# Kernel tuning notes

Measured on AMD Instinct MI355X. Metric: run time of the kernel, lower is better.

## Reference

```python
import jax, jax.numpy as jnp
import numpy as np
import math

M, N, D = 16384, 8192, 128
SIGMA = 1.0

def setup_inputs() -> dict:
    key = jax.random.key(0)
    k1, k2, k3 = jax.random.split(key, 3)
    x = jax.random.normal(k1, (M, D), dtype=jnp.float32)
    means = jax.random.normal(k2, (N, D), dtype=jnp.float32)
    weights = jax.random.uniform(k3, (N,), dtype=jnp.float32)
    return {"x": x, "means": means, "weights": weights}

def reference(x, means, weights):
    # GMM.eval_batch: cdist -> square -> gaussian kernel -> weighted sum
    var = SIGMA ** 2
    x = x.reshape(-1, means.shape[-1])
    x2 = jnp.sum(x * x, axis=-1, keepdims=True)            # (M,1)
    m2 = jnp.sum(means * means, axis=-1)                   # (N,)
    sq = jnp.maximum(x2 + m2[None, :] - 2.0 * (x @ means.T), 0.0)  # (M,N)
    coef = 1.0 / (2.0 * math.pi * var)
    dens = coef * jnp.exp(-sq / (2.0 * var))               # (M,N)
    return dens @ weights                                  # (M,)
```

## Files before the change

### kernel.cpp

```cpp
#include <hip/hip_runtime.h>
#include <math.h>

#define MM 16384
#define NN 8192
#define DD 128

#define L2E  1.4426950408889634f
#define COEF 0.15915494309189535f

__device__ __forceinline__ unsigned short f2h(float f) {
    _Float16 h = (_Float16)f;
    unsigned short u;
    __builtin_memcpy(&u, &h, 2);
    return u;
}

typedef __attribute__((ext_vector_type(8))) _Float16 f16x8;
typedef __attribute__((ext_vector_type(4))) float f32x4;

__global__ __launch_bounds__(256) void gmm_prep_f16(
    const float* __restrict__ x, const float* __restrict__ means,
    const float* __restrict__ w, short* __restrict__ Acat,
    short* __restrict__ Bcat, float* __restrict__ xc, float* __restrict__ mc)
{
    const int tid  = threadIdx.x;
    const int rbk  = blockIdx.x;
    const bool isx = rbk < (MM / 16);
    const int rb   = isx ? rbk : rbk - (MM / 16);
    const int lane = tid & 63;
    const int rp   = (tid >> 6) * 4 + (lane >> 4);
    const int cg   = lane & 15;
    const int p    = cg >> 2;
    const int gk   = cg & 3;
    const int row  = rb * 16 + rp;

    const float* src = (isx ? x : means) + (size_t)row * DD + cg * 8;
    float4 u0 = ((const float4*)src)[0];
    float4 u1 = ((const float4*)src)[1];
    float a[8] = {u0.x, u0.y, u0.z, u0.w, u1.x, u1.y, u1.z, u1.w};

    float ss = 0.f;
    unsigned hi[4];
    #pragma unroll
    for (int q = 0; q < 4; ++q) {
        ss = fmaf(a[2 * q], a[2 * q], fmaf(a[2 * q + 1], a[2 * q + 1], ss));
        float a0 = isx ? a[2 * q] * L2E     : a[2 * q];
        float a1 = isx ? a[2 * q + 1] * L2E : a[2 * q + 1];
        hi[q] = (unsigned)f2h(a0) | ((unsigned)f2h(a1) << 16);
    }
    uint4 HI = make_uint4(hi[0], hi[1], hi[2], hi[3]);

    const int slot = rp * 4 + ((gk + (rp >> 1)) & 3);
    short* base = (isx ? Acat : Bcat) + (size_t)rb * 2048 + p * 512 + slot * 8;
    *(uint4*)base = HI;

    ss += __shfl_xor(ss, 1, 16);
    ss += __shfl_xor(ss, 2, 16);
    ss += __shfl_xor(ss, 4, 16);
    ss += __shfl_xor(ss, 8, 16);
    if (cg == 0) {
        if (isx) xc[row] = -0.5f * ss * L2E;
        else     mc[row] = (logf(w[row]) - 0.5f * ss) * L2E;
    }
}

__global__ __launch_bounds__(256, 3) void gmm_mfma(
    const short* __restrict__ Acat, const short* __restrict__ Bcat,
    const float* __restrict__ xc, const float* __restrict__ mc,
    float* __restrict__ out)
{
    const int tid  = threadIdx.x;
    const int w    = tid >> 6, lane = tid & 63;
    const int wm   = w >> 1,   wn   = w & 1;
    const int quad = lane >> 4, col = lane & 15;
    const int m0   = blockIdx.x * 128;
    const int nb   = blockIdx.y * 128;

    const int rdo = col * 32 + ((quad + (col >> 1)) & 3) * 8;

    const short* ga = Acat + (size_t)(blockIdx.x * 8 + wm * 4) * 2048 + rdo;
    const short* gb = Bcat + (size_t)(blockIdx.y * 8 + wn * 4) * 2048 + rdo;

    float mcv[4];
    #pragma unroll
    for (int j = 0; j < 4; ++j) mcv[j] = mc[nb + wn * 64 + j * 16 + col];
    float xa[4][4];
    #pragma unroll
    for (int i = 0; i < 4; ++i) {
        float4 xv = *(const float4*)(xc + m0 + wm * 64 + i * 16 + quad * 4);
        xa[i][0] = xv.x; xa[i][1] = xv.y; xa[i][2] = xv.z; xa[i][3] = xv.w;
    }

    f32x4 acc[4][4];
    #pragma unroll
    for (int i = 0; i < 4; ++i)
        #pragma unroll
        for (int j = 0; j < 4; ++j)
            acc[i][j] = (f32x4){xa[i][0] + mcv[j], xa[i][1] + mcv[j],
                                xa[i][2] + mcv[j], xa[i][3] + mcv[j]};

    #pragma unroll
    for (int bk = 0; bk < 4; ++bk) {
        f16x8 af[4], bf[4];
        #pragma unroll
        for (int i = 0; i < 4; ++i)
            af[i] = *(const f16x8*)(ga + (size_t)i * 2048 + bk * 512);
        #pragma unroll
        for (int j = 0; j < 4; ++j)
            bf[j] = *(const f16x8*)(gb + (size_t)j * 2048 + bk * 512);
        #pragma unroll
        for (int j = 0; j < 4; ++j)
            #pragma unroll
            for (int i = 0; i < 4; ++i)
                acc[i][j] = __builtin_amdgcn_mfma_f32_16x16x32_f16(
                    af[i], bf[j], acc[i][j], 0, 0, 0);
    }

    #pragma unroll
    for (int i = 0; i < 4; ++i) {
        #pragma unroll
        for (int r = 0; r < 4; ++r) {
            float s = 0.f;
            #pragma unroll
            for (int j = 0; j < 4; ++j)
                s += __builtin_exp2f(acc[i][j][r]);
            s += __shfl_xor(s, 1, 16);
            s += __shfl_xor(s, 2, 16);
            s += __shfl_xor(s, 4, 16);
            s += __shfl_xor(s, 8, 16);
            if (col == 0)
                atomicAdd(out + m0 + wm * 64 + i * 16 + quad * 4 + r, COEF * s);
        }
    }
}

__global__ __launch_bounds__(256) void gmm_prep(
    const float* __restrict__ x, const float* __restrict__ means,
    const float* __restrict__ w, float* __restrict__ xc, float* __restrict__ mc)
{
    int tid = blockIdx.x * 256 + threadIdx.x;
    if (tid < MM) {
        const float4* row = (const float4*)(x + (size_t)tid * DD);
        float ss = 0.f;
        #pragma unroll
        for (int i = 0; i < DD / 4; ++i) {
            float4 v = row[i];
            ss = fmaf(v.x, v.x, fmaf(v.y, v.y, fmaf(v.z, v.z, fmaf(v.w, v.w, ss))));
        }
        xc[tid] = -0.5f * ss * L2E;
    } else if (tid < MM + NN) {
        int n = tid - MM;
        const float4* row = (const float4*)(means + (size_t)n * DD);
        float ss = 0.f;
        #pragma unroll
        for (int i = 0; i < DD / 4; ++i) {
            float4 v = row[i];
            ss = fmaf(v.x, v.x, fmaf(v.y, v.y, fmaf(v.z, v.z, fmaf(v.w, v.w, ss))));
        }
        mc[n] = (logf(w[n]) - 0.5f * ss) * L2E;
    }
}

__global__ __launch_bounds__(256, 2) void gmm_main(
    const float* __restrict__ x, const float* __restrict__ means,
    const float* __restrict__ xc, const float* __restrict__ mc,
    float* __restrict__ out)
{
    __shared__ __align__(16) float Asm[128 * 128];
    __shared__ __align__(16) float Bsm[2][16 * 128];

    const int t   = threadIdx.x;
    const int tc  = t & 15;
    const int tr  = t >> 4;
    const int r0  = blockIdx.x * 128;
    const int nq0 = blockIdx.y * 2048;

    {
        float4 tmp[16];
        #pragma unroll
        for (int ii = 0; ii < 16; ++ii) {
            int idx = t + ii * 256;
            int r   = idx >> 5;
            int k0  = (idx & 31) << 2;
            tmp[ii] = *(const float4*)(x + (size_t)(r0 + r) * DD + k0);
        }
        #pragma unroll
        for (int ii = 0; ii < 16; ++ii) {
            int idx = t + ii * 256;
            int r   = idx >> 5;
            int k0  = (idx & 31) << 2;
            int rb  = r >> 3, rl = r & 7;
            float v[4] = {tmp[ii].x, tmp[ii].y, tmp[ii].z, tmp[ii].w};
            #pragma unroll
            for (int j = 0; j < 4; ++j) {
                int k = k0 + j;
                Asm[k * 128 + (((rb ^ (k & 15)) << 3) | rl)] = v[j];
            }
        }
    }

    float xcv[8];
    {
        float4 a = *(const float4*)(xc + r0 + tr * 8);
        float4 b = *(const float4*)(xc + r0 + tr * 8 + 4);
        xcv[0] = a.x; xcv[1] = a.y; xcv[2] = a.z; xcv[3] = a.w;
        xcv[4] = b.x; xcv[5] = b.y; xcv[6] = b.z; xcv[7] = b.w;
    }

    float rowAcc[8];
    #pragma unroll
    for (int i = 0; i < 8; ++i) rowAcc[i] = 0.f;

    for (int ntile = 0; ntile < 16; ++ntile) {
        const int nbase = nq0 + ntile * 128;

        float acc[8][8];
        #pragma unroll
        for (int i = 0; i < 8; ++i)
            #pragma unroll
            for (int j = 0; j < 8; ++j) acc[i][j] = 0.f;

        float4 ld[2];
        #pragma unroll
        for (int ii = 0; ii < 2; ++ii) {
            int flat = t + ii * 256;
            int nl   = flat >> 2;
            int kl   = (flat & 3) << 2;
            ld[ii] = *(const float4*)(means + (size_t)(nbase + nl) * DD + kl);
        }

        for (int ks = 0; ks < 8; ++ks) {
            const int buf = ks & 1;
            #pragma unroll
            for (int ii = 0; ii < 2; ++ii) {
                int flat = t + ii * 256;
                int nl   = flat >> 2;
                int k0   = (flat & 3) << 2;
                int nbk  = nl >> 3, nll = nl & 7;
                float v[4] = {ld[ii].x, ld[ii].y, ld[ii].z, ld[ii].w};
                #pragma unroll
                for (int j = 0; j < 4; ++j) {
                    int kl = k0 + j;
                    Bsm[buf][kl * 128 + (((nbk ^ kl) << 3) | nll)] = v[j];
                }
            }
            if (ks < 7) {
                #pragma unroll
                for (int ii = 0; ii < 2; ++ii) {
                    int flat = t + ii * 256;
                    int nl   = flat >> 2;
                    int kl   = (flat & 3) << 2;
                    ld[ii] = *(const float4*)(means + (size_t)(nbase + nl) * DD
                                              + (ks + 1) * 16 + kl);
                }
            }
            __syncthreads();

            #pragma unroll
            for (int kk = 0; kk < 16; ++kk) {
                const int k = ks * 16 + kk;
                const float* apx = &Asm[k * 128 + ((tr ^ kk) << 3)];
                float4 a0 = *(const float4*)apx;
                float4 a1 = *(const float4*)(apx + 4);
                const float* bpx = &Bsm[buf][kk * 128 + ((tc ^ kk) << 3)];
                float4 b0 = *(const float4*)bpx;
                float4 b1 = *(const float4*)(bpx + 4);
                float av[8] = {a0.x, a0.y, a0.z, a0.w, a1.x, a1.y, a1.z, a1.w};
                float bv[8] = {b0.x, b0.y, b0.z, b0.w, b1.x, b1.y, b1.z, b1.w};
                #pragma unroll
                for (int i = 0; i < 8; ++i)
                    #pragma unroll
                    for (int j = 0; j < 8; ++j)
                        acc[i][j] = fmaf(av[i], bv[j], acc[i][j]);
            }
        }

        float mcv[8];
        {
            float4 a = *(const float4*)(mc + nbase + tc * 8);
            float4 b = *(const float4*)(mc + nbase + tc * 8 + 4);
            mcv[0] = a.x; mcv[1] = a.y; mcv[2] = a.z; mcv[3] = a.w;
            mcv[4] = b.x; mcv[5] = b.y; mcv[6] = b.z; mcv[7] = b.w;
        }
        #pragma unroll
        for (int i = 0; i < 8; ++i) {
            float s = 0.f;
            #pragma unroll
            for (int j = 0; j < 8; ++j) {
                float arg = fmaf(acc[i][j], L2E, xcv[i] + mcv[j]);
                s += __builtin_exp2f(arg);
            }
            rowAcc[i] += s;
        }
    }

    #pragma unroll
    for (int i = 0; i < 8; ++i) {
        float v = rowAcc[i];
        v += __shfl_xor(v, 1, 16);
        v += __shfl_xor(v, 2, 16);
        v += __shfl_xor(v, 4, 16);
        v += __shfl_xor(v, 8, 16);
        if (tc == 0) atomicAdd(out + r0 + tr * 8 + i, COEF * v);
    }
}

extern "C" void kernel_launch(void* const* d_in, const int* in_sizes, int n_in,
                              void* d_out, int out_size, void* d_ws, size_t ws_size,
                              hipStream_t stream) {
    const float* x     = (const float*)d_in[0];
    const float* means = (const float*)d_in[1];
    const float* w     = (const float*)d_in[2];
    float* out = (float*)d_out;

    const size_t needA = (size_t)MM * 128 * sizeof(short);
    const size_t needB = (size_t)NN * 128 * sizeof(short);
    const size_t need  = needA + needB + (size_t)(MM + NN) * 4;

    if (ws_size >= need) {
        short* Acat = (short*)d_ws;
        short* Bcat = Acat + (size_t)MM * 128;
        float* xc   = (float*)(Bcat + (size_t)NN * 128);
        float* mc   = xc + MM;
        hipMemsetAsync(out, 0, MM * sizeof(float), stream);
        gmm_prep_f16<<<(MM + NN) / 16, 256, 0, stream>>>(x, means, w, Acat, Bcat, xc, mc);
        gmm_mfma<<<dim3(MM / 128, NN / 128), 256, 0, stream>>>(Acat, Bcat, xc, mc, out);
    } else {
        float* xc = (float*)d_ws;
        float* mc = xc + MM;
        hipMemsetAsync(out, 0, MM * sizeof(float), stream);
        gmm_prep<<<(MM + NN + 255) / 256, 256, 0, stream>>>(x, means, w, xc, mc);
        gmm_main<<<dim3(MM / 128, 4), 256, 0, stream>>>(x, means, xc, mc, out);
    }
}
```

Before: 140.3 us.

## Stage MFMA operands through triple-buffered LDS with async global loads

The MFMA kernel now uses 512-thread blocks that each cover 128 rows by 1024 means. Operand chunks are streamed through a triple-buffered LDS ring filled by global_load_lds async copies, with vmcnt waits and barriers between stages. Per-row exp sums build up in registers across 8 N-tiles, which cuts the atomicAdd count by a factor of 8 and shares A/B tiles across waves. The cost is a block-wide barrier at every step, 48KB of LDS per block, and fewer blocks in the grid.

```diff
diff --git a/kernel.cpp b/kernel.cpp
--- a/kernel.cpp
+++ b/kernel.cpp
@@ -13,6 +13,13 @@
     unsigned short u;
     __builtin_memcpy(&u, &h, 2);
     return u;
+}
+
+__device__ __forceinline__ void async16(short* lds, const short* g) {
+    __builtin_amdgcn_global_load_lds(
+        (const __attribute__((address_space(1))) unsigned int*)g,
+        (__attribute__((address_space(3))) unsigned int*)lds,
+        16, 0, 0);
 }
 
 typedef __attribute__((ext_vector_type(8))) _Float16 f16x8;
@@ -64,74 +71,123 @@
     }
 }
 
-__global__ __launch_bounds__(256, 3) void gmm_mfma(
+__global__ __launch_bounds__(512, 4) void gmm_mfma(
     const short* __restrict__ Acat, const short* __restrict__ Bcat,
     const float* __restrict__ xc, const float* __restrict__ mc,
     float* __restrict__ out)
 {
+    __shared__ __align__(16) short smem[24576];
+
+#define AS(b) (smem + (b) * 4096)
+#define BS(b) (smem + 12288 + (b) * 4096)
+
     const int tid  = threadIdx.x;
     const int w    = tid >> 6, lane = tid & 63;
-    const int wm   = w >> 1,   wn   = w & 1;
+    const int wm   = w >> 2,   wn   = w & 3;
     const int quad = lane >> 4, col = lane & 15;
     const int m0   = blockIdx.x * 128;
-    const int nb   = blockIdx.y * 128;
-
-    const int rdo = col * 32 + ((quad + (col >> 1)) & 3) * 8;
-
-    const short* ga = Acat + (size_t)(blockIdx.x * 8 + wm * 4) * 2048 + rdo;
-    const short* gb = Bcat + (size_t)(blockIdx.y * 8 + wn * 4) * 2048 + rdo;
-
-    float mcv[4];
-    #pragma unroll
-    for (int j = 0; j < 4; ++j) mcv[j] = mc[nb + wn * 64 + j * 16 + col];
+    const int nb   = blockIdx.y * 1024;
+
+    const short* ga = Acat + (size_t)(blockIdx.x * 8 + w) * 2048 + lane * 8;
+    const short* gb = Bcat + (size_t)(blockIdx.y * 64 + w) * 2048 + lane * 8;
+    const int ofs = w * 512;
+
+    float mcv[8][2];
+    #pragma unroll
+    for (int nt = 0; nt < 8; ++nt)
+        #pragma unroll
+        for (int j = 0; j < 2; ++j)
+            mcv[nt][j] = mc[nb + nt * 128 + wn * 32 + j * 16 + col];
     float xa[4][4];
     #pragma unroll
     for (int i = 0; i < 4; ++i) {
         float4 xv = *(const float4*)(xc + m0 + wm * 64 + i * 16 + quad * 4);
         xa[i][0] = xv.x; xa[i][1] = xv.y; xa[i][2] = xv.z; xa[i][3] = xv.w;
     }
-
-    f32x4 acc[4][4];
+    float rowAcc[4][4];
     #pragma unroll
     for (int i = 0; i < 4; ++i)
         #pragma unroll
-        for (int j = 0; j < 4; ++j)
-            acc[i][j] = (f32x4){xa[i][0] + mcv[j], xa[i][1] + mcv[j],
-                                xa[i][2] + mcv[j], xa[i][3] + mcv[j]};
-
-    #pragma unroll
-    for (int bk = 0; bk < 4; ++bk) {
-        f16x8 af[4], bf[4];
-        #pragma unroll
-        for (int i = 0; i < 4; ++i)
-            af[i] = *(const f16x8*)(ga + (size_t)i * 2048 + bk * 512);
-        #pragma unroll
-        for (int j = 0; j < 4; ++j)
-            bf[j] = *(const f16x8*)(gb + (size_t)j * 2048 + bk * 512);
-        #pragma unroll
-        for (int j = 0; j < 4; ++j)
+        for (int r = 0; r < 4; ++r) rowAcc[i][r] = 0.f;
+
+    asm volatile("s_waitcnt vmcnt(0)" ::: "memory");
+    __builtin_amdgcn_sched_barrier(0);
+
+    async16(AS(0) + ofs, ga);
+    async16(BS(0) + ofs, gb);
+    async16(AS(1) + ofs, ga + 512);
+    async16(BS(1) + ofs, gb + 512);
+
+    const int rdo = col * 32 + ((quad + (col >> 1)) & 3) * 8;
+
+    f32x4 acc[4][2];
+
+    #pragma unroll
+    for (int p = 0; p < 32; ++p) {
+        const int nt = p >> 2, ck = p & 3;
+        if (p < 31) { asm volatile("s_waitcnt vmcnt(2)" ::: "memory"); }
+        else        { asm volatile("s_waitcnt vmcnt(0)" ::: "memory"); }
+        __builtin_amdgcn_sched_barrier(0);
+        __builtin_amdgcn_s_barrier();
+        __builtin_amdgcn_sched_barrier(0);
+        if (p + 2 < 32) {
+            const int g = p + 2, b = g % 3, gnt = g >> 2, gck = g & 3;
+            async16(AS(b) + ofs, ga + gck * 512);
+            async16(BS(b) + ofs, gb + (size_t)gnt * 16384 + gck * 512);
+        }
+        if (ck == 0) {
             #pragma unroll
             for (int i = 0; i < 4; ++i)
-                acc[i][j] = __builtin_amdgcn_mfma_f32_16x16x32_f16(
-                    af[i], bf[j], acc[i][j], 0, 0, 0);
+                #pragma unroll
+                for (int j = 0; j < 2; ++j)
+                    acc[i][j] = (f32x4){xa[i][0] + mcv[nt][j],
+                                        xa[i][1] + mcv[nt][j],
+                                        xa[i][2] + mcv[nt][j],
+                                        xa[i][3] + mcv[nt][j]};
+        }
+        {
+            const int cb = p % 3;
+            const short* as = AS(cb);
+            const short* bs = BS(cb);
+            f16x8 af[4];
+            #pragma unroll
+            for (int i = 0; i < 4; ++i)
+                af[i] = *(const f16x8*)(as + (wm * 4 + i) * 512 + rdo);
+            #pragma unroll
+            for (int j = 0; j < 2; ++j) {
+                f16x8 bfr = *(const f16x8*)(&bs[(wn * 2 + j) * 512 + rdo]);
+                #pragma unroll
+                for (int i = 0; i < 4; ++i)
+                    acc[i][j] = __builtin_amdgcn_mfma_f32_16x16x32_f16(
+                        af[i], bfr, acc[i][j], 0, 0, 0);
+            }
+        }
+        if (ck == 3) {
+            #pragma unroll
+            for (int i = 0; i < 4; ++i)
+                #pragma unroll
+                for (int r = 0; r < 4; ++r)
+                    rowAcc[i][r] += __builtin_exp2f(acc[i][0][r])
+                                  + __builtin_exp2f(acc[i][1][r]);
+        }
     }
 
     #pragma unroll
     for (int i = 0; i < 4; ++i) {
         #pragma unroll
         for (int r = 0; r < 4; ++r) {
-            float s = 0.f;
-            #pragma unroll
-            for (int j = 0; j < 4; ++j)
-                s += __builtin_exp2f(acc[i][j][r]);
-            s += __shfl_xor(s, 1, 16);
-            s += __shfl_xor(s, 2, 16);
-            s += __shfl_xor(s, 4, 16);
-            s += __shfl_xor(s, 8, 16);
+            float v = rowAcc[i][r];
+            v += __shfl_xor(v, 1, 16);
+            v += __shfl_xor(v, 2, 16);
+            v += __shfl_xor(v, 4, 16);
+            v += __shfl_xor(v, 8, 16);
             if (col == 0)
-                atomicAdd(out + m0 + wm * 64 + i * 16 + quad * 4 + r, COEF * s);
-        }
-    }
+                atomicAdd(out + m0 + wm * 64 + i * 16 + quad * 4 + r,
+                          COEF * v);
+        }
+    }
+#undef AS
+#undef BS
 }
 
 __global__ __launch_bounds__(256) void gmm_prep(
@@ -324,7 +380,7 @@
         float* mc   = xc + MM;
         hipMemsetAsync(out, 0, MM * sizeof(float), stream);
         gmm_prep_f16<<<(MM + NN) / 16, 256, 0, stream>>>(x, means, w, Acat, Bcat, xc, mc);
-        gmm_mfma<<<dim3(MM / 128, NN / 128), 256, 0, stream>>>(Acat, Bcat, xc, mc, out);
+        gmm_mfma<<<dim3(MM / 128, NN / 1024), 512, 0, stream>>>(Acat, Bcat, xc, mc, out);
     } else {
         float* xc = (float*)d_ws;
         float* mc = xc + MM;
```

Result: slower. 249.4 us (+77.8%).
